# Optimization experiments

Hardware: AMD Instinct MI355X
Metric: run time of the kernel (lower is better)

## Reference

```python
import jax, jax.numpy as jnp
import numpy as np


def _gcn_conv(x, W, b, src, dst, n):
    # x: [N, F_in] -> project first (dense GEMM), then normalized scatter-add.
    h = x @ W  # [N, F_out]
    deg = jax.ops.segment_sum(jnp.ones_like(dst, dtype=h.dtype), dst, num_segments=n)  # in-degree incl. self loops
    inv_sqrt = jax.lax.rsqrt(deg)  # deg >= 1 because self loops were added
    norm = inv_sqrt[src] * inv_sqrt[dst]  # [E+N]
    out = jax.ops.segment_sum(h[src] * norm[:, None], dst, num_segments=n)  # [N, F_out]
    return out + b


def setup_inputs() -> dict:
    key = jax.random.key(0)
    k1, k2, k3, k4 = jax.random.split(key, 4)
    N, E, F_IN, H, C = 10000, 160000, 3703, 1024, 6
    x = jax.random.normal(k1, (N, F_IN), dtype=jnp.float32)
    edge_index = jax.random.randint(k2, (2, E), 0, N, dtype=jnp.int64)
    # Glorot-style init for weights
    W1 = jax.random.normal(k3, (F_IN, H), dtype=jnp.float32) * np.float32(1.0 / np.sqrt(F_IN))
    W2 = jax.random.normal(k4, (H, C), dtype=jnp.float32) * np.float32(1.0 / np.sqrt(H))
    b1 = jnp.zeros((H,), dtype=jnp.float32)
    b2 = jnp.zeros((C,), dtype=jnp.float32)
    return {"x": x, "edge_index": edge_index, "W1": W1, "b1": b1, "W2": W2, "b2": b2}


def reference(x, edge_index, W1, b1, W2, b2):
    n = x.shape[0]
    # GCNConv adds self loops; degree normalization D^{-1/2}(A+I)D^{-1/2}
    loop = jnp.arange(n, dtype=edge_index.dtype)
    src = jnp.concatenate([edge_index[0], loop])
    dst = jnp.concatenate([edge_index[1], loop])
    h = _gcn_conv(x, W1, b1, src, dst, n)
    h = jax.nn.relu(h)
    # dropout is identity in eval mode
    h = _gcn_conv(h, W2, b2, src, dst, n)
    return jax.nn.log_softmax(h, axis=1)
```

## Files before the change

### kernel.cpp

```cpp
#include <hip/hip_runtime.h>
#include <stdint.h>

typedef unsigned short u16;
typedef unsigned int u32;
typedef __bf16 bf16x8 __attribute__((ext_vector_type(8)));
typedef float f32x4 __attribute__((ext_vector_type(4)));

#define N_NODES 10000
#define N_EDGES 160000
#define F_IN    3703
#define HDIM    1024
#define CDIM    6
#define MP      10112
#define KP      3712
#define KT      58

static __device__ __forceinline__ u16 f2bf(float f) {
    u32 u = __builtin_bit_cast(u32, f);
    u32 r = (u + 0x7fffu + ((u >> 16) & 1u)) >> 16;
    return (u16)r;
}
static __device__ __forceinline__ float bf2f(u16 b) {
    return __builtin_bit_cast(float, ((u32)b) << 16);
}

#define GL2LDS(g, l) __builtin_amdgcn_global_load_lds(                         \
    (const __attribute__((address_space(1))) void*)(g),                        \
    (__attribute__((address_space(3))) void*)(l), 16, 0, 0)

__global__ void k_count(const int* __restrict__ ei, int* counts) {
    int e = blockIdx.x * 256 + threadIdx.x;
    if (e < N_EDGES) {
        int dst = ei[N_EDGES + e];
        atomicAdd(&counts[dst], 1);
    }
}

__global__ void k_scan(const int* __restrict__ counts, int* __restrict__ offsets,
                       float* __restrict__ inv_sqrt) {
    __shared__ int wsum[16];
    int t = threadIdx.x, lane = t & 63, wv = t >> 6;
    int local[10];
    int s = 0;
    #pragma unroll
    for (int i = 0; i < 10; i++) {
        int idx = t * 10 + i;
        int v = (idx < N_NODES) ? counts[idx] : 0;
        local[i] = s; s += v;
    }
    int incl = s;
    #pragma unroll
    for (int off = 1; off < 64; off <<= 1) {
        int v = __shfl_up(incl, off);
        if (lane >= off) incl += v;
    }
    if (lane == 63) wsum[wv] = incl;
    __syncthreads();
    if (t == 0) {
        int a = 0;
        #pragma unroll
        for (int i = 0; i < 16; i++) { int v = wsum[i]; wsum[i] = a; a += v; }
    }
    __syncthreads();
    int base = wsum[wv] + incl - s;
    #pragma unroll
    for (int i = 0; i < 10; i++) {
        int idx = t * 10 + i;
        if (idx < N_NODES) {
            offsets[idx] = base + local[i];
            inv_sqrt[idx] = rsqrtf((float)(counts[idx] + 1));
        }
    }
    if (t == 1023) offsets[N_NODES] = wsum[15] + incl;
}

__global__ void k_fill(const int* __restrict__ ei, const int* __restrict__ offsets,
                       int* cursor, int* __restrict__ edge_src) {
    int e = blockIdx.x * 256 + threadIdx.x;
    if (e < N_EDGES) {
        int src = ei[e];
        int dst = ei[N_EDGES + e];
        int pos = atomicAdd(&cursor[dst], 1);
        edge_src[offsets[dst] + pos] = src;
    }
}

__global__ void k_cvt_x(const float* __restrict__ x, u16* __restrict__ A) {
    const int KP4 = KP / 4;
    int i = blockIdx.x * 256 + threadIdx.x;
    if (i >= MP * KP4) return;
    int m = i / KP4;
    int k4 = (i - m * KP4) * 4;
    float v0 = 0.f, v1 = 0.f, v2 = 0.f, v3 = 0.f;
    if (m < N_NODES) {
        const float* xp = x + (size_t)m * F_IN;
        if (k4 + 3 < F_IN) {
            v0 = xp[k4]; v1 = xp[k4 + 1]; v2 = xp[k4 + 2]; v3 = xp[k4 + 3];
        } else {
            if (k4     < F_IN) v0 = xp[k4];
            if (k4 + 1 < F_IN) v1 = xp[k4 + 1];
            if (k4 + 2 < F_IN) v2 = xp[k4 + 2];
            if (k4 + 3 < F_IN) v3 = xp[k4 + 3];
        }
    }
    ushort4 o;
    o.x = f2bf(v0); o.y = f2bf(v1); o.z = f2bf(v2); o.w = f2bf(v3);
    *(ushort4*)&A[(size_t)m * KP + k4] = o;
}

__global__ void k_cvt_w1t(const float* __restrict__ W1, u16* __restrict__ BT) {
    __shared__ u16 tile[64][66];
    int k0 = blockIdx.x * 64, n0 = blockIdx.y * 64;
    int tx = threadIdx.x & 63, ty = threadIdx.x >> 6;
    #pragma unroll
    for (int i = 0; i < 16; i++) {
        int kk = ty + i * 4;
        int k = k0 + kk;
        float v = (k < F_IN) ? W1[(size_t)k * HDIM + n0 + tx] : 0.f;
        tile[kk][tx] = f2bf(v);
    }
    __syncthreads();
    #pragma unroll
    for (int i = 0; i < 16; i++) {
        int nn = ty + i * 4;
        BT[(size_t)(n0 + nn) * KP + k0 + tx] = tile[tx][nn];
    }
}

__global__ __launch_bounds__(256) void k_gemm1(const u16* __restrict__ A,
                                               const u16* __restrict__ BT,
                                               u16* __restrict__ H1) {
    __shared__ __align__(16) u16 As[128 * 64];
    __shared__ __align__(16) u16 Bs[128 * 64];
    const int tid = threadIdx.x;
    const int lane = tid & 63;
    const int wid = tid >> 6;
    const int wm = wid >> 1, wn = wid & 1;

    const u32 orig = (u32)blockIdx.y * 8u + (u32)blockIdx.x;
    const u32 lin  = (orig & 7u) * 79u + (orig >> 3);
    const int bm = (int)(lin >> 3);
    const int bn = (int)(lin & 7u);

    int srow[4], scol[4], sdst[4];
    #pragma unroll
    for (int j = 0; j < 4; j++) {
        int q = wid * 4 + j;
        int e = q * 512 + lane * 8;
        int row = e >> 6, c = e & 63;
        srow[j] = row;
        scol[j] = c ^ ((row & 7) << 3);
        sdst[j] = q * 512;
    }
    const u16* Abase = A + (size_t)bm * 128 * KP;
    const u16* Bbase = BT + (size_t)bn * 128 * KP;

    f32x4 acc[4][4];
    #pragma unroll
    for (int i = 0; i < 4; i++)
        #pragma unroll
        for (int j = 0; j < 4; j++)
            acc[i][j] = (f32x4)0.f;

    for (int kt = 0; kt < KT; ++kt) {
        const int k0 = kt * 64;
        #pragma unroll
        for (int j = 0; j < 4; j++)
            GL2LDS(Abase + srow[j] * KP + k0 + scol[j], As + sdst[j]);
        #pragma unroll
        for (int j = 0; j < 4; j++)
            GL2LDS(Bbase + srow[j] * KP + k0 + scol[j], Bs + sdst[j]);
        __syncthreads();

        const int rA = wm * 64 + (lane & 15);
        const int rB = wn * 64 + (lane & 15);
        const int cb = (lane >> 4) << 3;
        #pragma unroll
        for (int kk = 0; kk < 2; kk++) {
            bf16x8 av[4], bv[4];
            const int cc = kk * 32 + cb;
            #pragma unroll
            for (int i = 0; i < 4; i++) {
                int r = rA + i * 16;
                av[i] = *(const bf16x8*)(As + r * 64 + (cc ^ ((r & 7) << 3)));
                int r2 = rB + i * 16;
                bv[i] = *(const bf16x8*)(Bs + r2 * 64 + (cc ^ ((r2 & 7) << 3)));
            }
            #pragma unroll
            for (int i = 0; i < 4; i++)
                #pragma unroll
                for (int j = 0; j < 4; j++)
                    acc[i][j] = __builtin_amdgcn_mfma_f32_16x16x32_bf16(
                        av[i], bv[j], acc[i][j], 0, 0, 0);
        }
        __syncthreads();
    }

    const int cr = (lane >> 4) * 4;
    const int ccol = lane & 15;
    #pragma unroll
    for (int i = 0; i < 4; i++) {
        #pragma unroll
        for (int j = 0; j < 4; j++) {
            #pragma unroll
            for (int r = 0; r < 4; r++) {
                int row = bm * 128 + wm * 64 + i * 16 + cr + r;
                if (row < N_NODES) {
                    int col = bn * 128 + wn * 64 + j * 16 + ccol;
                    H1[(size_t)row * HDIM + col] = f2bf(acc[i][j][r]);
                }
            }
        }
    }
}

__global__ void k_agg1g2(const u16* __restrict__ H1, const int* __restrict__ offsets,
                         const int* __restrict__ edge_src, const float* __restrict__ inv_sqrt,
                         const float* __restrict__ b1, const float* __restrict__ W2,
                         float* __restrict__ H2) {
    __shared__ float red[4][8];
    int node = blockIdx.x;
    int t = threadIdx.x;
    int lane = t & 63, wv = t >> 6;
    int f = t * 4;
    float is_n = inv_sqrt[node];
    float a0, a1, a2, a3;
    {
        float w = is_n * is_n;
        ushort4 v = *(const ushort4*)(H1 + (size_t)node * HDIM + f);
        a0 = bf2f(v.x) * w; a1 = bf2f(v.y) * w; a2 = bf2f(v.z) * w; a3 = bf2f(v.w) * w;
    }
    int beg = offsets[node], end = offsets[node + 1];
    for (int base = beg; base < end; base += 64) {
        int idx = base + lane;
        int sv = (idx < end) ? edge_src[idx] : 0;
        float pv = (idx < end) ? inv_sqrt[sv] : 0.f;
        int cnt = min(64, end - base);
        for (int i = 0; i < cnt; i++) {
            int s = __shfl(sv, i);
            float w = __shfl(pv, i) * is_n;
            ushort4 v = *(const ushort4*)(H1 + (size_t)s * HDIM + f);
            a0 += bf2f(v.x) * w; a1 += bf2f(v.y) * w;
            a2 += bf2f(v.z) * w; a3 += bf2f(v.w) * w;
        }
    }
    float4 bb = *(const float4*)(b1 + f);
    float z0 = fmaxf(a0 + bb.x, 0.f);
    float z1 = fmaxf(a1 + bb.y, 0.f);
    float z2 = fmaxf(a2 + bb.z, 0.f);
    float z3 = fmaxf(a3 + bb.w, 0.f);
    float acc[6];
    #pragma unroll
    for (int c = 0; c < 6; c++)
        acc[c] = z0 * W2[(size_t)f * 6 + c] + z1 * W2[(size_t)(f + 1) * 6 + c]
               + z2 * W2[(size_t)(f + 2) * 6 + c] + z3 * W2[(size_t)(f + 3) * 6 + c];
    #pragma unroll
    for (int c = 0; c < 6; c++) {
        #pragma unroll
        for (int off = 32; off > 0; off >>= 1) acc[c] += __shfl_xor(acc[c], off);
    }
    if (lane == 0) {
        #pragma unroll
        for (int c = 0; c < 6; c++) red[wv][c] = acc[c];
    }
    __syncthreads();
    if (t < 6) {
        float s = red[0][t] + red[1][t] + red[2][t] + red[3][t];
        H2[(size_t)node * CDIM + t] = s;
    }
}

__global__ void k_agg2(const float* __restrict__ H2, const int* __restrict__ offsets,
                       const int* __restrict__ edge_src, const float* __restrict__ inv_sqrt,
                       const float* __restrict__ b2, float* __restrict__ out) {
    int gt = blockIdx.x * 256 + threadIdx.x;
    int node = gt >> 3, sub = gt & 7;
    if (node >= N_NODES) return;
    float is_n = inv_sqrt[node];
    float acc[6] = {0.f, 0.f, 0.f, 0.f, 0.f, 0.f};
    int beg = offsets[node], end = offsets[node + 1];
    for (int e = beg + sub; e < end; e += 8) {
        int s = edge_src[e];
        float w = inv_sqrt[s] * is_n;
        #pragma unroll
        for (int c = 0; c < 6; c++) acc[c] += H2[(size_t)s * CDIM + c] * w;
    }
    if (sub == 0) {
        float w = is_n * is_n;
        #pragma unroll
        for (int c = 0; c < 6; c++) acc[c] += H2[(size_t)node * CDIM + c] * w;
    }
    #pragma unroll
    for (int off = 1; off < 8; off <<= 1) {
        #pragma unroll
        for (int c = 0; c < 6; c++) acc[c] += __shfl_xor(acc[c], off);
    }
    if (sub == 0) {
        float z[6];
        #pragma unroll
        for (int c = 0; c < 6; c++) z[c] = acc[c] + b2[c];
        float m = z[0];
        #pragma unroll
        for (int c = 1; c < 6; c++) m = fmaxf(m, z[c]);
        float ssum = 0.f;
        #pragma unroll
        for (int c = 0; c < 6; c++) ssum += __expf(z[c] - m);
        float l = m + logf(ssum);
        #pragma unroll
        for (int c = 0; c < 6; c++) out[(size_t)node * CDIM + c] = z[c] - l;
    }
}

extern "C" void kernel_launch(void* const* d_in, const int* in_sizes, int n_in,
                              void* d_out, int out_size, void* d_ws, size_t ws_size,
                              hipStream_t stream) {
    const float* x  = (const float*)d_in[0];
    const int*   ei = (const int*)d_in[1];
    const float* W1 = (const float*)d_in[2];
    const float* b1 = (const float*)d_in[3];
    const float* W2 = (const float*)d_in[4];
    const float* b2 = (const float*)d_in[5];
    float* out = (float*)d_out;

    char* ws = (char*)d_ws;
    size_t off = 0;
    auto alloc = [&](size_t bytes) -> void* {
        void* p = ws + off;
        off += (bytes + 255) & ~(size_t)255;
        return p;
    };
    u16* A        = (u16*)alloc((size_t)MP * KP * 2);
    u16* BT       = (u16*)alloc((size_t)HDIM * KP * 2);
    u16* H1       = (u16*)alloc((size_t)N_NODES * HDIM * 2);
    int* counts   = (int*)alloc(N_NODES * 4);
    int* cursor   = (int*)alloc(N_NODES * 4);
    int* offsets  = (int*)alloc((N_NODES + 1) * 4);
    float* inv_sq = (float*)alloc(N_NODES * 4);
    int* edge_src = (int*)alloc(N_EDGES * 4);
    float* H2 = (float*)BT;

    hipMemsetAsync(counts, 0, N_NODES * 4, stream);
    hipMemsetAsync(cursor, 0, N_NODES * 4, stream);
    k_count<<<(N_EDGES + 255) / 256, 256, 0, stream>>>(ei, counts);
    k_scan<<<1, 1024, 0, stream>>>(counts, offsets, inv_sq);
    k_fill<<<(N_EDGES + 255) / 256, 256, 0, stream>>>(ei, offsets, cursor, edge_src);

    k_cvt_x<<<(MP * (KP / 4) + 255) / 256, 256, 0, stream>>>(x, A);
    dim3 gT(KP / 64, HDIM / 64);
    k_cvt_w1t<<<gT, 256, 0, stream>>>(W1, BT);

    dim3 gG(HDIM / 128, 79);
    k_gemm1<<<gG, 256, 0, stream>>>(A, BT, H1);

    k_agg1g2<<<N_NODES, 256, 0, stream>>>(H1, offsets, edge_src, inv_sq, b1, W2, H2);
    k_agg2<<<(N_NODES * 8 + 255) / 256, 256, 0, stream>>>(H2, offsets, edge_src, inv_sq, b2, out);
}
```

Baseline: 241.8 us.

## Split layer-1 aggregation into per-node feature chunks with separate partial reduction

The fused aggregation+W2 kernel now launches one 64-thread block per (node, 128-feature chunk) instead of one 256-thread block per node. Each lane handles 2 features and reads edge indices directly rather than through shuffles, and the block writes partial 6-wide products. A new small kernel sums the 8 partials per node. The aim is more independent blocks and better latency hiding for the gather, at the cost of redundant edge-index and inv_sqrt loads per chunk, narrower per-thread loads, and an extra launch.

```diff
diff --git a/kernel.cpp b/kernel.cpp
--- a/kernel.cpp
+++ b/kernel.cpp
@@ -214,60 +214,58 @@
     }
 }
 
-__global__ void k_agg1g2(const u16* __restrict__ H1, const int* __restrict__ offsets,
-                         const int* __restrict__ edge_src, const float* __restrict__ inv_sqrt,
-                         const float* __restrict__ b1, const float* __restrict__ W2,
-                         float* __restrict__ H2) {
-    __shared__ float red[4][8];
-    int node = blockIdx.x;
-    int t = threadIdx.x;
-    int lane = t & 63, wv = t >> 6;
-    int f = t * 4;
-    float is_n = inv_sqrt[node];
-    float a0, a1, a2, a3;
+__global__ __launch_bounds__(64) void k_agg1g2(const u16* __restrict__ H1,
+                                               const int* __restrict__ offsets,
+                                               const int* __restrict__ edge_src,
+                                               const float* __restrict__ inv_sqrt,
+                                               const float* __restrict__ b1,
+                                               const float* __restrict__ W2,
+                                               float* __restrict__ H2p) {
+    const int b = blockIdx.x;
+    const int node = b >> 3, ch = b & 7;
+    const int t = threadIdx.x;
+    const int f = ch * 128 + t * 2;
+    const float is_n = inv_sqrt[node];
+    float a0, a1;
     {
         float w = is_n * is_n;
-        ushort4 v = *(const ushort4*)(H1 + (size_t)node * HDIM + f);
-        a0 = bf2f(v.x) * w; a1 = bf2f(v.y) * w; a2 = bf2f(v.z) * w; a3 = bf2f(v.w) * w;
-    }
-    int beg = offsets[node], end = offsets[node + 1];
-    for (int base = beg; base < end; base += 64) {
-        int idx = base + lane;
-        int sv = (idx < end) ? edge_src[idx] : 0;
-        float pv = (idx < end) ? inv_sqrt[sv] : 0.f;
-        int cnt = min(64, end - base);
-        for (int i = 0; i < cnt; i++) {
-            int s = __shfl(sv, i);
-            float w = __shfl(pv, i) * is_n;
-            ushort4 v = *(const ushort4*)(H1 + (size_t)s * HDIM + f);
-            a0 += bf2f(v.x) * w; a1 += bf2f(v.y) * w;
-            a2 += bf2f(v.z) * w; a3 += bf2f(v.w) * w;
-        }
-    }
-    float4 bb = *(const float4*)(b1 + f);
-    float z0 = fmaxf(a0 + bb.x, 0.f);
-    float z1 = fmaxf(a1 + bb.y, 0.f);
-    float z2 = fmaxf(a2 + bb.z, 0.f);
-    float z3 = fmaxf(a3 + bb.w, 0.f);
+        ushort2 v = *(const ushort2*)(H1 + (size_t)node * HDIM + f);
+        a0 = bf2f(v.x) * w; a1 = bf2f(v.y) * w;
+    }
+    const int beg = offsets[node], end = offsets[node + 1];
+    for (int e = beg; e < end; ++e) {
+        int s = edge_src[e];
+        float w = inv_sqrt[s] * is_n;
+        ushort2 v = *(const ushort2*)(H1 + (size_t)s * HDIM + f);
+        a0 += bf2f(v.x) * w;
+        a1 += bf2f(v.y) * w;
+    }
+    float z0 = fmaxf(a0 + b1[f], 0.f);
+    float z1 = fmaxf(a1 + b1[f + 1], 0.f);
     float acc[6];
     #pragma unroll
     for (int c = 0; c < 6; c++)
-        acc[c] = z0 * W2[(size_t)f * 6 + c] + z1 * W2[(size_t)(f + 1) * 6 + c]
-               + z2 * W2[(size_t)(f + 2) * 6 + c] + z3 * W2[(size_t)(f + 3) * 6 + c];
+        acc[c] = z0 * W2[(size_t)f * 6 + c] + z1 * W2[(size_t)(f + 1) * 6 + c];
     #pragma unroll
     for (int c = 0; c < 6; c++) {
         #pragma unroll
         for (int off = 32; off > 0; off >>= 1) acc[c] += __shfl_xor(acc[c], off);
     }
-    if (lane == 0) {
-        #pragma unroll
-        for (int c = 0; c < 6; c++) red[wv][c] = acc[c];
-    }
-    __syncthreads();
-    if (t < 6) {
-        float s = red[0][t] + red[1][t] + red[2][t] + red[3][t];
-        H2[(size_t)node * CDIM + t] = s;
-    }
+    if (t == 0) {
+        #pragma unroll
+        for (int c = 0; c < 6; c++) H2p[(size_t)b * 6 + c] = acc[c];
+    }
+}
+
+__global__ void k_h2red(const float* __restrict__ H2p, float* __restrict__ H2) {
+    int i = blockIdx.x * 256 + threadIdx.x;
+    if (i >= N_NODES * CDIM) return;
+    int node = i / CDIM, c = i - node * CDIM;
+    const float* p = H2p + (size_t)node * 48 + c;
+    float s = 0.f;
+    #pragma unroll
+    for (int ch = 0; ch < 8; ch++) s += p[ch * 6];
+    H2[i] = s;
 }
 
 __global__ void k_agg2(const float* __restrict__ H2, const int* __restrict__ offsets,
@@ -337,6 +335,7 @@
     int* offsets  = (int*)alloc((N_NODES + 1) * 4);
     float* inv_sq = (float*)alloc(N_NODES * 4);
     int* edge_src = (int*)alloc(N_EDGES * 4);
+    float* H2p    = (float*)alloc((size_t)N_NODES * 8 * CDIM * 4);
     float* H2 = (float*)BT;
 
     hipMemsetAsync(counts, 0, N_NODES * 4, stream);
@@ -352,6 +351,7 @@
     dim3 gG(HDIM / 128, 79);
     k_gemm1<<<gG, 256, 0, stream>>>(A, BT, H1);
 
-    k_agg1g2<<<N_NODES, 256, 0, stream>>>(H1, offsets, edge_src, inv_sq, b1, W2, H2);
+    k_agg1g2<<<N_NODES * 8, 64, 0, stream>>>(H1, offsets, edge_src, inv_sq, b1, W2, H2p);
+    k_h2red<<<(N_NODES * CDIM + 255) / 256, 256, 0, stream>>>(H2p, H2);
     k_agg2<<<(N_NODES * 8 + 255) / 256, 256, 0, stream>>>(H2, offsets, edge_src, inv_sq, b2, out);
 }
```

New measurement: 244.6 us. No clear change (+1.2%).

## Fuse fp32-to-bf16 conversion of x into the first GEMM's A-tile loads

Applied to the files above, without the earlier changes.

Removes the separate kernel that converted and padded x into a bf16 buffer. The GEMM now streams fp32 x straight into LDS with global_load_lds, using clamped flat indices in place of padding, and converts to bf16 in registers before the MFMAs. This drops a full read and write pass over the large input. In exchange the A tile in LDS doubles in size, each K-step does extra conversion work, and fp32 A data is re-read by every column block. Reads past the row end pick up the next row's values, which relies on W1's zero-padded K rows to cancel them.

```diff
diff --git a/kernel.cpp b/kernel.cpp
--- a/kernel.cpp
+++ b/kernel.cpp
@@ -11,7 +11,6 @@
 #define F_IN    3703
 #define HDIM    1024
 #define CDIM    6
-#define MP      10112
 #define KP      3712
 #define KT      58
 
@@ -85,29 +84,6 @@
     }
 }
 
-__global__ void k_cvt_x(const float* __restrict__ x, u16* __restrict__ A) {
-    const int KP4 = KP / 4;
-    int i = blockIdx.x * 256 + threadIdx.x;
-    if (i >= MP * KP4) return;
-    int m = i / KP4;
-    int k4 = (i - m * KP4) * 4;
-    float v0 = 0.f, v1 = 0.f, v2 = 0.f, v3 = 0.f;
-    if (m < N_NODES) {
-        const float* xp = x + (size_t)m * F_IN;
-        if (k4 + 3 < F_IN) {
-            v0 = xp[k4]; v1 = xp[k4 + 1]; v2 = xp[k4 + 2]; v3 = xp[k4 + 3];
-        } else {
-            if (k4     < F_IN) v0 = xp[k4];
-            if (k4 + 1 < F_IN) v1 = xp[k4 + 1];
-            if (k4 + 2 < F_IN) v2 = xp[k4 + 2];
-            if (k4 + 3 < F_IN) v3 = xp[k4 + 3];
-        }
-    }
-    ushort4 o;
-    o.x = f2bf(v0); o.y = f2bf(v1); o.z = f2bf(v2); o.w = f2bf(v3);
-    *(ushort4*)&A[(size_t)m * KP + k4] = o;
-}
-
 __global__ void k_cvt_w1t(const float* __restrict__ W1, u16* __restrict__ BT) {
     __shared__ u16 tile[64][66];
     int k0 = blockIdx.x * 64, n0 = blockIdx.y * 64;
@@ -127,10 +103,10 @@
     }
 }
 
-__global__ __launch_bounds__(256) void k_gemm1(const u16* __restrict__ A,
+__global__ __launch_bounds__(256) void k_gemm1(const float* __restrict__ x,
                                                const u16* __restrict__ BT,
                                                u16* __restrict__ H1) {
-    __shared__ __align__(16) u16 As[128 * 64];
+    __shared__ __align__(16) float Asf[128 * 64];
     __shared__ __align__(16) u16 Bs[128 * 64];
     const int tid = threadIdx.x;
     const int lane = tid & 63;
@@ -142,17 +118,28 @@
     const int bm = (int)(lin >> 3);
     const int bn = (int)(lin & 7u);
 
-    int srow[4], scol[4], sdst[4];
+    u32 aflat[8]; int adst[8];
+    #pragma unroll
+    for (int j = 0; j < 8; j++) {
+        int q = wid * 8 + j;
+        int e = q * 256 + lane * 4;
+        int row = e >> 6, c = e & 63;
+        int csrc = c ^ ((row & 7) << 3);
+        aflat[j] = (u32)(bm * 128 + row) * F_IN + csrc;
+        adst[j] = q * 256;
+    }
+    const u32 XMAX = (u32)N_NODES * F_IN - 4;
+
+    int srowB[4], scolB[4], sdstB[4];
     #pragma unroll
     for (int j = 0; j < 4; j++) {
         int q = wid * 4 + j;
         int e = q * 512 + lane * 8;
         int row = e >> 6, c = e & 63;
-        srow[j] = row;
-        scol[j] = c ^ ((row & 7) << 3);
-        sdst[j] = q * 512;
-    }
-    const u16* Abase = A + (size_t)bm * 128 * KP;
+        srowB[j] = row;
+        scolB[j] = c ^ ((row & 7) << 3);
+        sdstB[j] = q * 512;
+    }
     const u16* Bbase = BT + (size_t)bn * 128 * KP;
 
     f32x4 acc[4][4];
@@ -165,11 +152,14 @@
     for (int kt = 0; kt < KT; ++kt) {
         const int k0 = kt * 64;
         #pragma unroll
+        for (int j = 0; j < 8; j++) {
+            u32 flat = aflat[j] + (u32)k0;
+            flat = flat > XMAX ? XMAX : flat;
+            GL2LDS(x + flat, Asf + adst[j]);
+        }
+        #pragma unroll
         for (int j = 0; j < 4; j++)
-            GL2LDS(Abase + srow[j] * KP + k0 + scol[j], As + sdst[j]);
-        #pragma unroll
-        for (int j = 0; j < 4; j++)
-            GL2LDS(Bbase + srow[j] * KP + k0 + scol[j], Bs + sdst[j]);
+            GL2LDS(Bbase + (size_t)srowB[j] * KP + k0 + scolB[j], Bs + sdstB[j]);
         __syncthreads();
 
         const int rA = wm * 64 + (lane & 15);
@@ -182,7 +172,16 @@
             #pragma unroll
             for (int i = 0; i < 4; i++) {
                 int r = rA + i * 16;
-                av[i] = *(const bf16x8*)(As + r * 64 + (cc ^ ((r & 7) << 3)));
+                int pos = r * 64 + (cc ^ ((r & 7) << 3));
+                f32x4 lo = *(const f32x4*)(Asf + pos);
+                f32x4 hi = *(const f32x4*)(Asf + pos + 4);
+                bf16x8 a;
+                #pragma unroll
+                for (int m = 0; m < 4; m++) {
+                    a[m]     = (__bf16)lo[m];
+                    a[m + 4] = (__bf16)hi[m];
+                }
+                av[i] = a;
                 int r2 = rB + i * 16;
                 bv[i] = *(const bf16x8*)(Bs + r2 * 64 + (cc ^ ((r2 & 7) << 3)));
             }
@@ -329,7 +328,6 @@
         off += (bytes + 255) & ~(size_t)255;
         return p;
     };
-    u16* A        = (u16*)alloc((size_t)MP * KP * 2);
     u16* BT       = (u16*)alloc((size_t)HDIM * KP * 2);
     u16* H1       = (u16*)alloc((size_t)N_NODES * HDIM * 2);
     int* counts   = (int*)alloc(N_NODES * 4);
@@ -345,12 +343,11 @@
     k_scan<<<1, 1024, 0, stream>>>(counts, offsets, inv_sq);
     k_fill<<<(N_EDGES + 255) / 256, 256, 0, stream>>>(ei, offsets, cursor, edge_src);
 
-    k_cvt_x<<<(MP * (KP / 4) + 255) / 256, 256, 0, stream>>>(x, A);
     dim3 gT(KP / 64, HDIM / 64);
     k_cvt_w1t<<<gT, 256, 0, stream>>>(W1, BT);
 
     dim3 gG(HDIM / 128, 79);
-    k_gemm1<<<gG, 256, 0, stream>>>(A, BT, H1);
+    k_gemm1<<<gG, 256, 0, stream>>>(x, BT, H1);
 
     k_agg1g2<<<N_NODES, 256, 0, stream>>>(H1, offsets, edge_src, inv_sq, b1, W2, H2);
     k_agg2<<<(N_NODES * 8 + 255) / 256, 256, 0, stream>>>(H2, offsets, edge_src, inv_sq, b2, out);
```

Measured after the change: 249.5 us. 3.2% more time.
